# Performance work log

Hardware: AMD Instinct MI355X
Metric: run time of the kernel (lower is better)

Reference implementation:

```python
import jax, jax.numpy as jnp
import numpy as np

NUM_HEADS = 12


def setup_inputs() -> dict:
    key = jax.random.key(0)
    k0, k1, k2 = jax.random.split(key, 3)
    B, S, D = 2, 2048, 1536
    scale = 1.0 / np.sqrt(D)
    return {
        "hidden_states": jax.random.normal(k0, (B, S, D), dtype=jnp.float32),
        "W_fc": jax.random.normal(k1, (D, D), dtype=jnp.float32) * scale,
        "b_fc": jnp.zeros((D,), dtype=jnp.float32),
        "W_proj": jax.random.normal(k2, (D, D), dtype=jnp.float32) * scale,
        "b_proj": jnp.zeros((D,), dtype=jnp.float32),
    }


def reference(hidden_states, W_fc, b_fc, W_proj, b_proj):
    B, S, D = hidden_states.shape
    H = NUM_HEADS
    hd = D // H
    # value_states: [B, H, S, hd] (key_states == value_states in the original)
    v = (hidden_states @ W_fc.T + b_fc).reshape(B, S, H, hd).transpose(0, 2, 1, 3)
    # Uniform-weight causal sliding-window attention, window_h = 2^(h+1)-1.
    i = jnp.arange(S)[:, None]          # query pos
    j = jnp.arange(S)[None, :]          # key pos
    w = (2 ** jnp.arange(1, H + 1, dtype=jnp.int32) - 1)[:, None, None]  # [H,1,1]
    mask = (j <= i) & (j >= i - w + 1)                                    # [H,S,S]
    valid_len = jnp.minimum(i + 1, w).astype(v.dtype)                     # [H,S,1]
    attn = jnp.where(mask, 1.0 / valid_len, 0.0)                          # [H,S,S]
    # [H,S,S] x [B,H,S,hd] -> [B,S,H,hd] -> [B,S,D]
    out = jnp.einsum("hqk,bhkd->bqhd", attn, v).reshape(B, S, D)
    attn_weights = jnp.broadcast_to(attn[None], (B, H, S, S))
    return out @ W_proj.T + b_proj, attn_weights
```

## Files before the change

### kernel.cpp

```cpp
#include <hip/hip_runtime.h>
#include <hip/hip_bf16.h>

#define S_LEN   2048
#define DMODEL  1536
#define NBATCH  2
#define NHEADS  12
#define MROWS   (NBATCH * S_LEN)
#define NCHUNK  64
#define CHUNK   32

#define NGEMM_BLK  384
#define AW_BLK     3072
#define AW_TOTAL4  25165824u
#define AW_HALF4   12582912u

typedef unsigned short u16;
typedef __attribute__((ext_vector_type(8))) short bf16x8;
typedef __attribute__((ext_vector_type(4))) float f32x4;

__device__ __forceinline__ u16 f2bf(float x) {
  unsigned u = __float_as_uint(x);
  u += 0x7fffu + ((u >> 16) & 1u);
  return (u16)(u >> 16);
}
__device__ __forceinline__ float bf2f(u16 x) {
  return __uint_as_float(((unsigned)x) << 16);
}

#define N4_HID  1572864
#define N4_W    589824
__global__ void cvt_all(const float4* __restrict__ h, const float4* __restrict__ wf,
                        const float4* __restrict__ wp, ushort4* __restrict__ ho,
                        ushort4* __restrict__ wfo, ushort4* __restrict__ wpo) {
  int t = blockIdx.x * blockDim.x + threadIdx.x;
  const float4* src;
  ushort4* dst;
  int idx;
  if (t < N4_HID)            { src = h;  dst = ho;  idx = t; }
  else if (t < N4_HID + N4_W){ src = wf; dst = wfo; idx = t - N4_HID; }
  else                       { src = wp; dst = wpo; idx = t - N4_HID - N4_W; }
  float4 f = src[idx];
  ushort4 o;
  o.x = f2bf(f.x); o.y = f2bf(f.y); o.z = f2bf(f.z); o.w = f2bf(f.w);
  dst[idx] = o;
}

__device__ __forceinline__ void gld_lds16(u16* lds, const u16* g) {
  __builtin_amdgcn_global_load_lds(
      (const __attribute__((address_space(1))) unsigned int*)g,
      (__attribute__((address_space(3))) unsigned int*)lds, 16, 0, 0);
}

template <bool WITH_CSUM, typename CT>
__global__ __launch_bounds__(256)
void gemm_aw(const u16* __restrict__ A, const u16* __restrict__ B,
             const float* __restrict__ bias, CT* __restrict__ C,
             float* __restrict__ cs, f32x4* __restrict__ aw,
             unsigned aw0, unsigned awcnt, int Ndim, int Kdim) {
  if ((int)blockIdx.x >= NGEMM_BLK) {
    const unsigned stride = (gridDim.x - NGEMM_BLK) * 256u;
    const unsigned end = aw0 + awcnt;
    unsigned t = aw0 + (blockIdx.x - NGEMM_BLK) * 256u + threadIdx.x;
    for (; t < end; t += stride) {
      int j0 = (int)(t & 511u) << 2;
      int i  = (int)(t >> 9) & (S_LEN - 1);
      int bh = (int)(t >> 20);
      int h  = bh >= NHEADS ? bh - NHEADS : bh;
      int w  = (2 << h) - 1;
      int len = min(i + 1, w);
      float inv = 1.0f / (float)len;
      int lo = i - w + 1;
      f32x4 r;
      r.x = (j0     <= i && j0     >= lo) ? inv : 0.f;
      r.y = (j0 + 1 <= i && j0 + 1 >= lo) ? inv : 0.f;
      r.z = (j0 + 2 <= i && j0 + 2 >= lo) ? inv : 0.f;
      r.w = (j0 + 3 <= i && j0 + 3 >= lo) ? inv : 0.f;
      __builtin_nontemporal_store(r, &aw[t]);
    }
    return;
  }

  __shared__ __align__(16) u16 As[128 * 32];
  __shared__ __align__(16) u16 Bs[128 * 32];
  __shared__ float colpart[4][128];

  const int tid  = threadIdx.x;
  const int wave = tid >> 6;
  const int lane = tid & 63;
  const int l15  = lane & 15;
  const int quad = lane >> 4;
  const int bm = (blockIdx.x / (DMODEL / 128)) * 128;
  const int bn = (blockIdx.x % (DMODEL / 128)) * 128;
  const int wm = (wave >> 1) * 64;
  const int wn = (wave & 1) * 64;

  f32x4 acc[4][4] = {};

  const int srow = wave * 32 + (lane >> 2);
  const int skk  = (lane & 3) * 8;
  const u16* gA = A + (size_t)(bm + srow) * Kdim + skk;
  const u16* gB = B + (size_t)(bn + srow) * Kdim + skk;
  u16* lA = &As[(wave * 32) * 32];
  u16* lB = &Bs[(wave * 32) * 32];
  const size_t rstep16 = (size_t)16 * Kdim;

  for (int k0 = 0; k0 < Kdim; k0 += 32) {
    gld_lds16(lA,           gA + k0);
    gld_lds16(lA + 16 * 32, gA + k0 + rstep16);
    gld_lds16(lB,           gB + k0);
    gld_lds16(lB + 16 * 32, gB + k0 + rstep16);
    __syncthreads();

    bf16x8 af[4], bfr[4];
#pragma unroll
    for (int i = 0; i < 4; ++i)
      af[i] = *(const bf16x8*)&As[(wm + i * 16 + l15) * 32 + quad * 8];
#pragma unroll
    for (int j = 0; j < 4; ++j)
      bfr[j] = *(const bf16x8*)&Bs[(wn + j * 16 + l15) * 32 + quad * 8];
#pragma unroll
    for (int i = 0; i < 4; ++i)
#pragma unroll
      for (int j = 0; j < 4; ++j)
        acc[i][j] = __builtin_amdgcn_mfma_f32_16x16x32_bf16(af[i], bfr[j], acc[i][j], 0, 0, 0);
    __syncthreads();
  }

  const int r0 = quad * 4;
#pragma unroll
  for (int j = 0; j < 4; ++j) {
    const int col = bn + wn + j * 16 + l15;
    const float bj = bias[col];
    float sA = 0.f, sB = 0.f;
#pragma unroll
    for (int i = 0; i < 4; ++i) {
      const int row = bm + wm + i * 16 + r0;
#pragma unroll
      for (int r = 0; r < 4; ++r) {
        float cv = acc[i][j][r] + bj;
        if constexpr (sizeof(CT) == 2)
          C[(size_t)(row + r) * Ndim + col] = (CT)f2bf(cv);
        else
          C[(size_t)(row + r) * Ndim + col] = (CT)cv;
        if (WITH_CSUM) { if (i < 2) sA += cv; else sB += cv; }
      }
    }
    if (WITH_CSUM) {
      sA += __shfl_xor(sA, 16); sA += __shfl_xor(sA, 32);
      sB += __shfl_xor(sB, 16); sB += __shfl_xor(sB, 32);
      if (quad == 0) {
        colpart[(wm >> 5) | 0][wn + j * 16 + l15] = sA;
        colpart[(wm >> 5) | 1][wn + j * 16 + l15] = sB;
      }
    }
  }
  if (WITH_CSUM) {
    __syncthreads();
    if (tid < 128) {
      const int b  = bm >> 11;
      const int c0 = (bm & 2047) >> 5;
#pragma unroll
      for (int g = 0; g < 4; ++g)
        cs[((size_t)b * NCHUNK + c0 + g) * DMODEL + bn + tid] = colpart[g][tid];
    }
  }
}

__global__ void chunk_prefix(const float* __restrict__ cs, float* __restrict__ E) {
  int t = blockIdx.x * blockDim.x + threadIdx.x;
  int d = t % DMODEL;
  int c = (t / DMODEL) % NCHUNK;
  int b = t / (DMODEL * NCHUNK);
  const float* p = cs + (size_t)b * NCHUNK * DMODEL + d;
  float s = 0.f;
  for (int cc = 0; cc < c; ++cc) s += p[(size_t)cc * DMODEL];
  E[t] = s;
}

__global__ void winavg_strip(const u16* __restrict__ v, const float* __restrict__ E,
                             u16* __restrict__ A2) {
  int t = blockIdx.x * blockDim.x + threadIdx.x;
  int d = t % DMODEL;
  int s = (t / DMODEL) & 255;
  int b = t / (DMODEL * 256);
  const int h = d >> 7;
  const int w = (2 << h) - 1;
  const u16* vb  = v + (size_t)b * S_LEN * DMODEL + d;
  const float* Eb = E + (size_t)b * NCHUNK * DMODEL + d;

  const int i0 = s * 8;
  float lead = Eb[(size_t)(i0 >> 5) * DMODEL];
  for (int r = i0 & ~31; r < i0; ++r)
    lead += bf2f(vb[(size_t)r * DMODEL]);

  float trail = 0.f;
  if (i0 + 7 >= w) {
    const int jf = max(i0, w) - w;
    if (jf > 0) {
      const int ct = (jf - 1) >> 5;
      trail = Eb[(size_t)ct * DMODEL];
      for (int r = ct * 32; r < jf; ++r)
        trail += bf2f(vb[(size_t)r * DMODEL]);
    }
  }

  u16* out = A2 + ((size_t)(b * S_LEN + i0)) * DMODEL + d;
#pragma unroll
  for (int rr = 0; rr < 8; ++rr) {
    const int i = i0 + rr;
    lead += bf2f(vb[(size_t)i * DMODEL]);
    float o;
    if (i < w) {
      o = lead / (float)(i + 1);
    } else {
      trail += bf2f(vb[(size_t)(i - w) * DMODEL]);
      o = (lead - trail) / (float)w;
    }
    out[(size_t)rr * DMODEL] = f2bf(o);
  }
}

extern "C" void kernel_launch(void* const* d_in, const int* in_sizes, int n_in,
                              void* d_out, int out_size, void* d_ws, size_t ws_size,
                              hipStream_t stream) {
  const float* hidden = (const float*)d_in[0];
  const float* W_fc   = (const float*)d_in[1];
  const float* b_fc   = (const float*)d_in[2];
  const float* W_proj = (const float*)d_in[3];
  const float* b_proj = (const float*)d_in[4];
  float* outp = (float*)d_out;
  f32x4* aw = (f32x4*)(outp + (size_t)MROWS * DMODEL);

  char* ws = (char*)d_ws;
  u16*   A16   = (u16*)(ws);
  u16*   Wfc16 = (u16*)(ws + 12582912);
  u16*   Wpj16 = (u16*)(ws + 17301504);
  u16*   v16   = (u16*)(ws + 22020096);
  float* csums = (float*)(ws + 34603008);
  float* Epre  = (float*)(ws + 35389440);

  cvt_all<<<10752, 256, 0, stream>>>((const float4*)hidden, (const float4*)W_fc,
                                     (const float4*)W_proj, (ushort4*)A16,
                                     (ushort4*)Wfc16, (ushort4*)Wpj16);

  gemm_aw<true, u16><<<NGEMM_BLK + AW_BLK, 256, 0, stream>>>(
      A16, Wfc16, b_fc, v16, csums, aw, 0u, AW_HALF4, DMODEL, DMODEL);

  chunk_prefix<<<(NBATCH * NCHUNK * DMODEL) / 256, 256, 0, stream>>>(csums, Epre);

  winavg_strip<<<(NBATCH * (S_LEN / 8) * DMODEL) / 256, 256, 0, stream>>>(v16, Epre, A16);

  gemm_aw<false, float><<<NGEMM_BLK + AW_BLK, 256, 0, stream>>>(
      A16, Wpj16, b_proj, outp, nullptr, aw, AW_HALF4, AW_HALF4, DMODEL, DMODEL);
}
```

Measured before the change: 541.4 us.

## Double-buffer GEMM LDS loads and spread attention-weight writes across all kernels

Gives the GEMM K-loop two LDS buffers, so the global-to-LDS load of the next tile is issued before the MFMAs of the current tile run, and one barrier per iteration is dropped. The attention-weight fill, which writes about 400 MB, is split across all four kernels instead of only the two GEMMs. The prefix-sum and window-average kernels now carry extra blocks that write their share, so this bandwidth-bound work overlaps the lighter stages. The fp32 output of the second GEMM now uses nontemporal stores. The cost is doubled LDS use per block, which may lower occupancy.

```diff
diff --git a/kernel.cpp b/kernel.cpp
--- a/kernel.cpp
+++ b/kernel.cpp
@@ -12,7 +12,16 @@
 #define NGEMM_BLK  384
 #define AW_BLK     3072
 #define AW_TOTAL4  25165824u
-#define AW_HALF4   12582912u
+
+#define AW_G1   10223616u
+#define AW_PF    1572864u
+#define AW_WA    3932160u
+#define AW_G2    9437184u
+
+#define PF_BLK   768
+#define PF_AWBLK 1536
+#define WA_BLK   3072
+#define WA_AWBLK 1536
 
 typedef unsigned short u16;
 typedef __attribute__((ext_vector_type(8))) short bf16x8;
@@ -25,6 +34,29 @@
 }
 __device__ __forceinline__ float bf2f(u16 x) {
   return __uint_as_float(((unsigned)x) << 16);
+}
+
+__device__ __forceinline__ void aw_stream(f32x4* __restrict__ aw, unsigned aw0,
+                                          unsigned awcnt, unsigned blk, unsigned nblk) {
+  const unsigned stride = nblk * 256u;
+  const unsigned end = aw0 + awcnt;
+  unsigned t = aw0 + blk * 256u + threadIdx.x;
+  for (; t < end; t += stride) {
+    int j0 = (int)(t & 511u) << 2;
+    int i  = (int)(t >> 9) & (S_LEN - 1);
+    int bh = (int)(t >> 20);
+    int h  = bh >= NHEADS ? bh - NHEADS : bh;
+    int w  = (2 << h) - 1;
+    int len = min(i + 1, w);
+    float inv = 1.0f / (float)len;
+    int lo = i - w + 1;
+    f32x4 r;
+    r.x = (j0     <= i && j0     >= lo) ? inv : 0.f;
+    r.y = (j0 + 1 <= i && j0 + 1 >= lo) ? inv : 0.f;
+    r.z = (j0 + 2 <= i && j0 + 2 >= lo) ? inv : 0.f;
+    r.w = (j0 + 3 <= i && j0 + 3 >= lo) ? inv : 0.f;
+    __builtin_nontemporal_store(r, &aw[t]);
+  }
 }
 
 #define N4_HID  1572864
@@ -58,30 +90,12 @@
              float* __restrict__ cs, f32x4* __restrict__ aw,
              unsigned aw0, unsigned awcnt, int Ndim, int Kdim) {
   if ((int)blockIdx.x >= NGEMM_BLK) {
-    const unsigned stride = (gridDim.x - NGEMM_BLK) * 256u;
-    const unsigned end = aw0 + awcnt;
-    unsigned t = aw0 + (blockIdx.x - NGEMM_BLK) * 256u + threadIdx.x;
-    for (; t < end; t += stride) {
-      int j0 = (int)(t & 511u) << 2;
-      int i  = (int)(t >> 9) & (S_LEN - 1);
-      int bh = (int)(t >> 20);
-      int h  = bh >= NHEADS ? bh - NHEADS : bh;
-      int w  = (2 << h) - 1;
-      int len = min(i + 1, w);
-      float inv = 1.0f / (float)len;
-      int lo = i - w + 1;
-      f32x4 r;
-      r.x = (j0     <= i && j0     >= lo) ? inv : 0.f;
-      r.y = (j0 + 1 <= i && j0 + 1 >= lo) ? inv : 0.f;
-      r.z = (j0 + 2 <= i && j0 + 2 >= lo) ? inv : 0.f;
-      r.w = (j0 + 3 <= i && j0 + 3 >= lo) ? inv : 0.f;
-      __builtin_nontemporal_store(r, &aw[t]);
-    }
+    aw_stream(aw, aw0, awcnt, blockIdx.x - NGEMM_BLK, gridDim.x - NGEMM_BLK);
     return;
   }
 
-  __shared__ __align__(16) u16 As[128 * 32];
-  __shared__ __align__(16) u16 Bs[128 * 32];
+  __shared__ __align__(16) u16 As[2][128 * 32];
+  __shared__ __align__(16) u16 Bs[2][128 * 32];
   __shared__ float colpart[4][128];
 
   const int tid  = threadIdx.x;
@@ -100,30 +114,38 @@
   const int skk  = (lane & 3) * 8;
   const u16* gA = A + (size_t)(bm + srow) * Kdim + skk;
   const u16* gB = B + (size_t)(bn + srow) * Kdim + skk;
-  u16* lA = &As[(wave * 32) * 32];
-  u16* lB = &Bs[(wave * 32) * 32];
+  const int lofs = (wave * 32) * 32;
   const size_t rstep16 = (size_t)16 * Kdim;
 
+  gld_lds16(&As[0][lofs],           gA);
+  gld_lds16(&As[0][lofs + 16 * 32], gA + rstep16);
+  gld_lds16(&Bs[0][lofs],           gB);
+  gld_lds16(&Bs[0][lofs + 16 * 32], gB + rstep16);
+
+  int cur = 0;
   for (int k0 = 0; k0 < Kdim; k0 += 32) {
-    gld_lds16(lA,           gA + k0);
-    gld_lds16(lA + 16 * 32, gA + k0 + rstep16);
-    gld_lds16(lB,           gB + k0);
-    gld_lds16(lB + 16 * 32, gB + k0 + rstep16);
     __syncthreads();
+    if (k0 + 32 < Kdim) {
+      const int nxt = cur ^ 1;
+      gld_lds16(&As[nxt][lofs],           gA + k0 + 32);
+      gld_lds16(&As[nxt][lofs + 16 * 32], gA + k0 + 32 + rstep16);
+      gld_lds16(&Bs[nxt][lofs],           gB + k0 + 32);
+      gld_lds16(&Bs[nxt][lofs + 16 * 32], gB + k0 + 32 + rstep16);
+    }
 
     bf16x8 af[4], bfr[4];
 #pragma unroll
     for (int i = 0; i < 4; ++i)
-      af[i] = *(const bf16x8*)&As[(wm + i * 16 + l15) * 32 + quad * 8];
+      af[i] = *(const bf16x8*)&As[cur][(wm + i * 16 + l15) * 32 + quad * 8];
 #pragma unroll
     for (int j = 0; j < 4; ++j)
-      bfr[j] = *(const bf16x8*)&Bs[(wn + j * 16 + l15) * 32 + quad * 8];
+      bfr[j] = *(const bf16x8*)&Bs[cur][(wn + j * 16 + l15) * 32 + quad * 8];
 #pragma unroll
     for (int i = 0; i < 4; ++i)
 #pragma unroll
       for (int j = 0; j < 4; ++j)
         acc[i][j] = __builtin_amdgcn_mfma_f32_16x16x32_bf16(af[i], bfr[j], acc[i][j], 0, 0, 0);
-    __syncthreads();
+    cur ^= 1;
   }
 
   const int r0 = quad * 4;
@@ -138,10 +160,11 @@
 #pragma unroll
       for (int r = 0; r < 4; ++r) {
         float cv = acc[i][j][r] + bj;
-        if constexpr (sizeof(CT) == 2)
+        if constexpr (sizeof(CT) == 2) {
           C[(size_t)(row + r) * Ndim + col] = (CT)f2bf(cv);
-        else
-          C[(size_t)(row + r) * Ndim + col] = (CT)cv;
+        } else {
+          __builtin_nontemporal_store((CT)cv, &C[(size_t)(row + r) * Ndim + col]);
+        }
         if (WITH_CSUM) { if (i < 2) sA += cv; else sB += cv; }
       }
     }
@@ -166,7 +189,12 @@
   }
 }
 
-__global__ void chunk_prefix(const float* __restrict__ cs, float* __restrict__ E) {
+__global__ void chunk_prefix_aw(const float* __restrict__ cs, float* __restrict__ E,
+                                f32x4* __restrict__ aw, unsigned aw0, unsigned awcnt) {
+  if ((int)blockIdx.x >= PF_BLK) {
+    aw_stream(aw, aw0, awcnt, blockIdx.x - PF_BLK, PF_AWBLK);
+    return;
+  }
   int t = blockIdx.x * blockDim.x + threadIdx.x;
   int d = t % DMODEL;
   int c = (t / DMODEL) % NCHUNK;
@@ -177,8 +205,13 @@
   E[t] = s;
 }
 
-__global__ void winavg_strip(const u16* __restrict__ v, const float* __restrict__ E,
-                             u16* __restrict__ A2) {
+__global__ void winavg_aw(const u16* __restrict__ v, const float* __restrict__ E,
+                          u16* __restrict__ A2,
+                          f32x4* __restrict__ aw, unsigned aw0, unsigned awcnt) {
+  if ((int)blockIdx.x >= WA_BLK) {
+    aw_stream(aw, aw0, awcnt, blockIdx.x - WA_BLK, WA_AWBLK);
+    return;
+  }
   int t = blockIdx.x * blockDim.x + threadIdx.x;
   int d = t % DMODEL;
   int s = (t / DMODEL) & 255;
@@ -244,12 +277,14 @@
                                      (ushort4*)Wfc16, (ushort4*)Wpj16);
 
   gemm_aw<true, u16><<<NGEMM_BLK + AW_BLK, 256, 0, stream>>>(
-      A16, Wfc16, b_fc, v16, csums, aw, 0u, AW_HALF4, DMODEL, DMODEL);
-
-  chunk_prefix<<<(NBATCH * NCHUNK * DMODEL) / 256, 256, 0, stream>>>(csums, Epre);
-
-  winavg_strip<<<(NBATCH * (S_LEN / 8) * DMODEL) / 256, 256, 0, stream>>>(v16, Epre, A16);
+      A16, Wfc16, b_fc, v16, csums, aw, 0u, AW_G1, DMODEL, DMODEL);
+
+  chunk_prefix_aw<<<PF_BLK + PF_AWBLK, 256, 0, stream>>>(
+      csums, Epre, aw, AW_G1, AW_PF);
+
+  winavg_aw<<<WA_BLK + WA_AWBLK, 256, 0, stream>>>(
+      v16, Epre, A16, aw, AW_G1 + AW_PF, AW_WA);
 
   gemm_aw<false, float><<<NGEMM_BLK + AW_BLK, 256, 0, stream>>>(
-      A16, Wpj16, b_proj, outp, nullptr, aw, AW_HALF4, AW_HALF4, DMODEL, DMODEL);
-}
+      A16, Wpj16, b_proj, outp, nullptr, aw, AW_G1 + AW_PF + AW_WA, AW_G2, DMODEL, DMODEL);
+}
```

Result: no change. 532.8 us (-1.6%).
